# Kernel optimization log

Measured on AMD Instinct MI355X. Metric: run time of the kernel, lower is better.

The kernel has to match this reference:

```python
import jax, jax.numpy as jnp
import numpy as np

N_HEADS = 16
ROPE_BASE = 10000.0


def _rope_cos_sin(seq_len, head_dim, dtype):
    half = head_dim // 2
    inv_freq = 1.0 / (ROPE_BASE ** (jnp.arange(0, half, dtype=jnp.float32) / half))
    ang = jnp.arange(seq_len, dtype=jnp.float32)[:, None] * inv_freq[None, :]  # [S, half]
    cos = jnp.concatenate([jnp.cos(ang), jnp.cos(ang)], axis=-1).astype(dtype)  # [S, hd]
    sin = jnp.concatenate([jnp.sin(ang), jnp.sin(ang)], axis=-1).astype(dtype)
    return cos, sin


def _rotate_half(x):
    half = x.shape[-1] // 2
    return jnp.concatenate([-x[..., half:], x[..., :half]], axis=-1)


def setup_inputs() -> dict:
    key = jax.random.key(0)
    k1, k2, k3 = jax.random.split(key, 3)
    B, S, D = 2, 2048, 1024
    x = jax.random.normal(k1, (B, S, D), dtype=jnp.float32)
    w_qkv = jax.random.normal(k2, (D, 3 * D), dtype=jnp.float32) * (1.0 / np.sqrt(D))
    w_out = jax.random.normal(k3, (D, D), dtype=jnp.float32) * (1.0 / np.sqrt(D))
    return {"x": x, "w_qkv": w_qkv, "w_out": w_out}


def reference(x, w_qkv, w_out):
    B, S, D = x.shape
    H = N_HEADS
    hd = D // H
    scale = 1.0 / np.sqrt(hd)

    qkv = x @ w_qkv  # [B, S, 3D]
    q, k, v = jnp.split(qkv, 3, axis=-1)
    # [B, H, S, hd]
    q = q.reshape(B, S, H, hd).transpose(0, 2, 1, 3)
    k = k.reshape(B, S, H, hd).transpose(0, 2, 1, 3)
    v = v.reshape(B, S, H, hd).transpose(0, 2, 1, 3)

    cos, sin = _rope_cos_sin(S, hd, x.dtype)  # [S, hd]
    q = q * cos + _rotate_half(q) * sin
    k = k * cos + _rotate_half(k) * sin

    scores = jnp.einsum("bhqd,bhkd->bhqk", q, k) * scale  # [B, H, S, S]
    causal = jnp.tril(jnp.ones((S, S), dtype=bool))
    scores = jnp.where(causal[None, None, :, :], scores, -jnp.inf)

    probs = jax.nn.softmax(scores.astype(jnp.float32), axis=-1).astype(q.dtype)
    out = jnp.einsum("bhqk,bhkd->bhqd", probs, v)  # [B, H, S, hd]
    out = out.transpose(0, 2, 1, 3).reshape(B, S, D)
    return out @ w_out
```

## Files before the change

kernel.cpp:

```cpp
#include <hip/hip_runtime.h>
#include <math.h>
#include <type_traits>

#define B_  2
#define S_  2048
#define D_  1024
#define H_  16

typedef short bf16x8 __attribute__((ext_vector_type(8)));
typedef short bf16x4 __attribute__((ext_vector_type(4)));
typedef float f32x4  __attribute__((ext_vector_type(4)));

__device__ __forceinline__ short f2bf(float f) {
    unsigned u = __builtin_bit_cast(unsigned, f);
    u += 0x7FFFu + ((u >> 16) & 1u);
    return (short)(u >> 16);
}
__device__ __forceinline__ float bf2f(short s) {
    unsigned u = ((unsigned)(unsigned short)s) << 16;
    return __builtin_bit_cast(float, u);
}

__device__ __forceinline__ void gload16(const short* g, const void* l) {
    __builtin_amdgcn_global_load_lds(
        (const __attribute__((address_space(1))) void*)g,
        (__attribute__((address_space(3))) void*)l, 16, 0, 0);
}

__global__ __launch_bounds__(256) void cvt_bf16_kernel(
    const float* __restrict__ in, short* __restrict__ out)
{
    int i = (blockIdx.x * 256 + threadIdx.x) * 8;
    float4 a = *(const float4*)(in + i);
    float4 b = *(const float4*)(in + i + 4);
    bf16x8 o;
    o[0] = f2bf(a.x); o[1] = f2bf(a.y); o[2] = f2bf(a.z); o[3] = f2bf(a.w);
    o[4] = f2bf(b.x); o[5] = f2bf(b.y); o[6] = f2bf(b.z); o[7] = f2bf(b.w);
    *(bf16x8*)(out + i) = o;
}

__global__ __launch_bounds__(256) void transpose_cvt_kernel(
    const float* __restrict__ in, short* __restrict__ out, int K, int N)
{
    __shared__ short t[64][72];
    const int k0 = blockIdx.y * 64, n0 = blockIdx.x * 64;
    const int r = threadIdx.x >> 2;
    const int c = (threadIdx.x & 3) * 16;
    const float* src = in + (size_t)(k0 + r) * N + n0 + c;
#pragma unroll
    for (int i = 0; i < 16; ++i) t[c + i][r] = f2bf(src[i]);
    __syncthreads();
    short* dst = out + (size_t)(n0 + r) * K + k0 + c;
    *(bf16x8*)(dst)     = *(const bf16x8*)&t[r][c];
    *(bf16x8*)(dst + 8) = *(const bf16x8*)&t[r][c + 8];
}

__global__ __launch_bounds__(256) void rope_tab_kernel(float2* __restrict__ tab)
{
    int idx = blockIdx.x * 256 + threadIdx.x;
    int j = idx & 31, s = idx >> 5;
    float inv = powf(10000.0f, -(float)j * (1.0f / 32.0f));
    float sn, cs;
    sincosf((float)s * inv, &sn, &cs);
    tab[idx] = make_float2(cs, sn);
}

__global__ __launch_bounds__(256) void gemm_bt_f32(
    const short* __restrict__ A, const short* __restrict__ Bt,
    float* __restrict__ C, int M, int N, int K)
{
    __shared__ short smem[18432];

    const int tid  = threadIdx.x;
    const int wave = tid >> 6, lane = tid & 63;
    const int quad = lane >> 4, l16 = lane & 15;
    const int wm = wave >> 1, wn = wave & 1;
    const int row0 = blockIdx.y * 128, col0 = blockIdx.x * 64;

    f32x4 acc[4][2];
#pragma unroll
    for (int mi = 0; mi < 4; ++mi)
#pragma unroll
        for (int ni = 0; ni < 2; ++ni) acc[mi][ni] = (f32x4)0.f;

    const int sr = tid >> 2;
    const int sc = (tid & 3) * 8;
    const short* a0 = A  + (size_t)(row0 + sr) * K + sc;
    const short* a1 = A  + (size_t)(row0 + 64 + sr) * K + sc;
    const short* b0 = Bt + (size_t)(col0 + sr) * K + sc;

    auto stage = [&](int b, int kt) {
        char* l = (char*)(smem + b * 6144) + wave * 1024;
        const int k0 = kt * 32;
        gload16(a0 + k0, l);
        gload16(a1 + k0, l + 4096);
        gload16(b0 + k0, l + 8192);
    };

    const int NT = K >> 5;
    stage(0, 0);
    stage(1, 1);
    int bufid = 0;
    for (int kt = 0; kt < NT; ++kt) {
        if (kt + 1 < NT) { asm volatile("s_waitcnt vmcnt(3)" ::: "memory"); }
        else             { asm volatile("s_waitcnt vmcnt(0)" ::: "memory"); }
        __builtin_amdgcn_s_barrier();
        __builtin_amdgcn_sched_barrier(0);
        if (kt + 2 < NT) {
            int nb = bufid + 2; if (nb >= 3) nb -= 3;
            stage(nb, kt + 2);
        }

        const short* As = smem + bufid * 6144;
        const short* Bs = As + 4096;
        bf16x8 af[4], bfr[2];
#pragma unroll
        for (int mi = 0; mi < 4; ++mi)
            af[mi] = *(const bf16x8*)(As + (wm * 64 + mi * 16 + l16) * 32 + quad * 8);
#pragma unroll
        for (int ni = 0; ni < 2; ++ni)
            bfr[ni] = *(const bf16x8*)(Bs + (wn * 32 + ni * 16 + l16) * 32 + quad * 8);
#pragma unroll
        for (int mi = 0; mi < 4; ++mi)
#pragma unroll
            for (int ni = 0; ni < 2; ++ni)
                acc[mi][ni] = __builtin_amdgcn_mfma_f32_16x16x32_bf16(
                    af[mi], bfr[ni], acc[mi][ni], 0, 0, 0);

        bufid = (bufid + 1 == 3) ? 0 : bufid + 1;
    }

#pragma unroll
    for (int mi = 0; mi < 4; ++mi)
#pragma unroll
        for (int ni = 0; ni < 2; ++ni)
#pragma unroll
            for (int r = 0; r < 4; ++r) {
                int row = row0 + wm * 64 + mi * 16 + quad * 4 + r;
                int col = col0 + wn * 32 + ni * 16 + l16;
                C[(size_t)row * N + col] = acc[mi][ni][r];
            }
}

__global__ __launch_bounds__(256) void gemm_qkv(
    const short* __restrict__ A, const short* __restrict__ Bt,
    const float2* __restrict__ tab,
    short* __restrict__ Qb, short* __restrict__ Kb, short* __restrict__ Vt)
{
    const int K = 1024;
    extern __shared__ short smem[];
    short* Sc = smem;

    const int tid  = threadIdx.x;
    const int wave = tid >> 6, lane = tid & 63;
    const int quad = lane >> 4, l16 = lane & 15;
    const int wm = wave >> 1, wn = wave & 1;
    const int row0 = blockIdx.y * 128, col0 = blockIdx.x * 128;

    f32x4 acc[4][4];
#pragma unroll
    for (int mi = 0; mi < 4; ++mi)
#pragma unroll
        for (int ni = 0; ni < 4; ++ni) acc[mi][ni] = (f32x4)0.f;

    const int sr = tid >> 2;
    const int sc = (tid & 3) * 8;
    const short* a0 = A  + (size_t)(row0 + sr) * K + sc;
    const short* a1 = A  + (size_t)(row0 + 64 + sr) * K + sc;
    const short* b0 = Bt + (size_t)(col0 + sr) * K + sc;
    const short* b1 = Bt + (size_t)(col0 + 64 + sr) * K + sc;

    auto stage = [&](int b, int kt) {
        char* l = (char*)(smem + b * 8192) + wave * 1024;
        const int k0 = kt * 32;
        gload16(a0 + k0, l);
        gload16(a1 + k0, l + 4096);
        gload16(b0 + k0, l + 8192);
        gload16(b1 + k0, l + 12288);
    };

    const int NT = K >> 5;
    stage(0, 0);
    stage(1, 1);
    int bufid = 0;
    for (int kt = 0; kt < NT; ++kt) {
        if (kt + 1 < NT) { asm volatile("s_waitcnt vmcnt(4)" ::: "memory"); }
        else             { asm volatile("s_waitcnt vmcnt(0)" ::: "memory"); }
        __builtin_amdgcn_s_barrier();
        __builtin_amdgcn_sched_barrier(0);
        if (kt + 2 < NT) {
            int nb = bufid + 2; if (nb >= 3) nb -= 3;
            stage(nb, kt + 2);
        }

        const short* As = smem + bufid * 8192;
        const short* Bs = As + 4096;
        bf16x8 af[4], bfr[4];
#pragma unroll
        for (int mi = 0; mi < 4; ++mi)
            af[mi] = *(const bf16x8*)(As + (wm * 64 + mi * 16 + l16) * 32 + quad * 8);
#pragma unroll
        for (int ni = 0; ni < 4; ++ni)
            bfr[ni] = *(const bf16x8*)(Bs + (wn * 64 + ni * 16 + l16) * 32 + quad * 8);
#pragma unroll
        for (int mi = 0; mi < 4; ++mi)
#pragma unroll
            for (int ni = 0; ni < 4; ++ni)
                acc[mi][ni] = __builtin_amdgcn_mfma_f32_16x16x32_bf16(
                    af[mi], bfr[ni], acc[mi][ni], 0, 0, 0);

        bufid = (bufid + 1 == 3) ? 0 : bufid + 1;
    }

    __syncthreads();

    const int sec  = (col0 + wn * 64) >> 6;
    const int h    = sec & 15;
    const int kind = sec >> 4;
    short* myS = Sc + wave * 4608;

    const int mrow0 = row0 + wm * 64;
    const int b  = mrow0 >> 11;
    const int bh = b * 16 + h;
    const int sbase = mrow0 & (S_ - 1);

    if (kind < 2) {
#pragma unroll
        for (int mi = 0; mi < 4; ++mi) {
#pragma unroll
            for (int r = 0; r < 4; ++r) {
                int sl = mi * 16 + quad * 4 + r;
                int s = sbase + sl;
#pragma unroll
                for (int ni = 0; ni < 2; ++ni) {
                    int j = ni * 16 + l16;
                    float2 t = tab[s * 32 + j];
                    float lo = acc[mi][ni][r], hi = acc[mi][ni + 2][r];
                    float olo = lo * t.x - hi * t.y;
                    float ohi = hi * t.x + lo * t.y;
                    if (kind == 0) { olo *= 0.125f; ohi *= 0.125f; }
                    myS[sl * 72 + j]      = f2bf(olo);
                    myS[sl * 72 + 32 + j] = f2bf(ohi);
                }
            }
        }
        const int rl = lane >> 3;
        const int cl = (lane & 7) * 8;
        short* dst = (kind == 0 ? Qb : Kb);
#pragma unroll
        for (int p = 0; p < 8; ++p) {
            int rr = p * 8 + rl;
            bf16x8 v = *(const bf16x8*)&myS[rr * 72 + cl];
            *(bf16x8*)(dst + ((size_t)bh * S_ + sbase + rr) * 64 + cl) = v;
        }
    } else {
#pragma unroll
        for (int mi = 0; mi < 4; ++mi)
#pragma unroll
            for (int ni = 0; ni < 4; ++ni) {
                bf16x4 p;
                p[0] = f2bf(acc[mi][ni][0]);
                p[1] = f2bf(acc[mi][ni][1]);
                p[2] = f2bf(acc[mi][ni][2]);
                p[3] = f2bf(acc[mi][ni][3]);
                *(bf16x4*)&myS[(ni * 16 + l16) * 72 + mi * 16 + quad * 4] = p;
            }
        const int rl = lane >> 3;
        const int cl = (lane & 7) * 8;
#pragma unroll
        for (int p = 0; p < 8; ++p) {
            int dd = p * 8 + rl;
            bf16x8 v = *(const bf16x8*)&myS[dd * 72 + cl];
            *(bf16x8*)(Vt + ((size_t)bh * 64 + dd) * S_ + sbase + cl) = v;
        }
    }
}

__global__ __launch_bounds__(128, 4) void attn_kernel(
    const short* __restrict__ Qb, const short* __restrict__ Kb,
    const short* __restrict__ Vt, short* __restrict__ Opart,
    float* __restrict__ lpart)
{
    __shared__ short Ps[64][72];

    const int lin = blockIdx.x;
    const int xcd = lin & 7;
    const int j   = lin >> 3;
    const int bh   = xcd * 4 + (j & 3);
    const int task = j >> 2;

    const int g = task < 8 ? 0 : task < 24 ? 1 : task < 48 ? 2 : 3;
    const int cumstart = g == 0 ? 0 : g == 1 ? 8 : g == 2 ? 24 : 48;
    const int idx = task - cumstart;
    const int qd = idx / (g + 1);
    const int qb = 8 * g + qd;
    const int c  = idx - qd * (g + 1);
    const int t0 = c * 8;
    const int t1 = min(qb, c * 8 + 7);

    const int wave = threadIdx.x >> 6, lane = threadIdx.x & 63;
    const int quad = lane >> 4, l16 = lane & 15;
    const size_t head64 = (size_t)bh * S_ * 64;

    bf16x8 qf[2][2];
#pragma unroll
    for (int m = 0; m < 2; ++m) {
        const short* qrow = Qb + head64
            + (size_t)(qb * 64 + wave * 32 + m * 16 + l16) * 64 + quad * 8;
        qf[m][0] = *(const bf16x8*)(qrow);
        qf[m][1] = *(const bf16x8*)(qrow + 32);
    }

    bf16x8 ones;
#pragma unroll
    for (int i = 0; i < 8; ++i) ones[i] = (short)0x3F80;

    f32x4 lacc[2] = {(f32x4)0.f, (f32x4)0.f};
    f32x4 oacc[2][4];
#pragma unroll
    for (int m = 0; m < 2; ++m)
#pragma unroll
        for (int nt = 0; nt < 4; ++nt) oacc[m][nt] = (f32x4)0.f;

    for (int t = t0; t <= t1; ++t) {
        const short* kb = Kb + head64 + (size_t)t * 64 * 64;
        const short* vb = Vt + head64 + t * 64;

        f32x4 s4[2][4];
#pragma unroll
        for (int nt = 0; nt < 4; ++nt) {
            const short* kr = kb + (nt * 16 + l16) * 64 + quad * 8;
            bf16x8 k0 = *(const bf16x8*)kr;
            bf16x8 k1 = *(const bf16x8*)(kr + 32);
#pragma unroll
            for (int m = 0; m < 2; ++m) {
                f32x4 a = (f32x4)0.f;
                a = __builtin_amdgcn_mfma_f32_16x16x32_bf16(k0, qf[m][0], a, 0, 0, 0);
                a = __builtin_amdgcn_mfma_f32_16x16x32_bf16(k1, qf[m][1], a, 0, 0, 0);
                s4[m][nt] = a;
            }
        }

        if (t == qb) {
#pragma unroll
            for (int m = 0; m < 2; ++m)
#pragma unroll
                for (int nt = 0; nt < 4; ++nt)
#pragma unroll
                    for (int r = 0; r < 4; ++r)
                        if (nt * 16 + quad * 4 + r > wave * 32 + m * 16 + l16)
                            s4[m][nt][r] = -INFINITY;
        }

#pragma unroll
        for (int m = 0; m < 2; ++m)
#pragma unroll
            for (int nt = 0; nt < 4; ++nt) {
                bf16x4 p;
#pragma unroll
                for (int r = 0; r < 4; ++r)
                    p[r] = f2bf(__expf(s4[m][nt][r] - 8.0f));
                *(bf16x4*)&Ps[wave * 32 + m * 16 + l16][nt * 16 + quad * 4] = p;
            }

        bf16x8 pa[2][2];
#pragma unroll
        for (int m = 0; m < 2; ++m) {
            pa[m][0] = *(const bf16x8*)&Ps[wave * 32 + m * 16 + l16][quad * 8];
            pa[m][1] = *(const bf16x8*)&Ps[wave * 32 + m * 16 + l16][32 + quad * 8];
        }

#pragma unroll
        for (int m = 0; m < 2; ++m) {
            lacc[m] = __builtin_amdgcn_mfma_f32_16x16x32_bf16(pa[m][0], ones, lacc[m], 0, 0, 0);
            lacc[m] = __builtin_amdgcn_mfma_f32_16x16x32_bf16(pa[m][1], ones, lacc[m], 0, 0, 0);
        }

#pragma unroll
        for (int nt = 0; nt < 4; ++nt) {
            const short* vrp = vb + (size_t)(nt * 16 + l16) * S_ + quad * 8;
            bf16x8 vb0 = *(const bf16x8*)vrp;
            bf16x8 vb1 = *(const bf16x8*)(vrp + 32);
#pragma unroll
            for (int m = 0; m < 2; ++m) {
                oacc[m][nt] = __builtin_amdgcn_mfma_f32_16x16x32_bf16(
                    pa[m][0], vb0, oacc[m][nt], 0, 0, 0);
                oacc[m][nt] = __builtin_amdgcn_mfma_f32_16x16x32_bf16(
                    pa[m][1], vb1, oacc[m][nt], 0, 0, 0);
            }
        }
    }

    const int pidx = bh * 80 + task;
#pragma unroll
    for (int m = 0; m < 2; ++m)
#pragma unroll
        for (int r = 0; r < 4; ++r) {
            int ql = wave * 32 + m * 16 + quad * 4 + r;
            short* orow = Opart + (size_t)pidx * 4096 + ql * 64;
#pragma unroll
            for (int nt = 0; nt < 4; ++nt)
                orow[nt * 16 + l16] = f2bf(oacc[m][nt][r]);
            if (l16 == 0)
                lpart[(size_t)pidx * 64 + ql] = lacc[m][r];
        }
}

__global__ __launch_bounds__(256) void combine_kernel(
    const short* __restrict__ Opart, const float* __restrict__ lpart,
    short* __restrict__ attnb)
{
    const int qb = blockIdx.x, bh = blockIdx.y;
    const int g = qb >> 3, nch = g + 1;
    const int cbase = bh * 80 + nch * (qb - 4 * g);
    const int q = threadIdx.x >> 2;
    const int dg = (threadIdx.x & 3) * 16;

    float lsum = 0.f;
    float acc[16];
#pragma unroll
    for (int i = 0; i < 16; ++i) acc[i] = 0.f;

    for (int cc = 0; cc < nch; ++cc) {
        lsum += lpart[(size_t)(cbase + cc) * 64 + q];
        const short* src = Opart + (size_t)(cbase + cc) * 4096 + q * 64 + dg;
        bf16x8 o0 = *(const bf16x8*)src;
        bf16x8 o1 = *(const bf16x8*)(src + 8);
#pragma unroll
        for (int i = 0; i < 8; ++i) {
            acc[i]     += bf2f(o0[i]);
            acc[i + 8] += bf2f(o1[i]);
        }
    }
    float inv = 1.0f / lsum;
    const int b = bh >> 4, h = bh & 15;
    bf16x8 r0, r1;
#pragma unroll
    for (int i = 0; i < 8; ++i) {
        r0[i] = f2bf(acc[i] * inv);
        r1[i] = f2bf(acc[i + 8] * inv);
    }
    short* dst = attnb + (size_t)(b * S_ + qb * 64 + q) * 1024 + h * 64 + dg;
    *(bf16x8*)dst       = r0;
    *(bf16x8*)(dst + 8) = r1;
}

extern "C" void kernel_launch(void* const* d_in, const int* in_sizes, int n_in,
                              void* d_out, int out_size, void* d_ws, size_t ws_size,
                              hipStream_t stream)
{
    const float* x     = (const float*)d_in[0];
    const float* w_qkv = (const float*)d_in[1];
    const float* w_out = (const float*)d_in[2];
    float* out = (float*)d_out;

    short* Qb   = (short*)d_ws;
    short* Kb   = Qb   + (size_t)4096 * 1024;
    short* Vt   = Kb   + (size_t)4096 * 1024;
    short* Xb   = Vt   + (size_t)4096 * 1024;
    short* Wqt  = Xb   + (size_t)4096 * 1024;
    short* Wot  = Wqt  + (size_t)3072 * 1024;
    float2* tab = (float2*)(Wot + (size_t)1024 * 1024);
    short* Opart = (short*)(tab + 2048 * 32);
    float* lbuf  = (float*)(Opart + (size_t)2560 * 4096);
    short* attnb = Xb;

    cvt_bf16_kernel<<<(4096 * 1024 / 8) / 256, 256, 0, stream>>>(x, Xb);
    transpose_cvt_kernel<<<dim3(3072 / 64, 1024 / 64), 256, 0, stream>>>(
        w_qkv, Wqt, 1024, 3072);
    transpose_cvt_kernel<<<dim3(1024 / 64, 1024 / 64), 256, 0, stream>>>(
        w_out, Wot, 1024, 1024);
    rope_tab_kernel<<<(2048 * 32) / 256, 256, 0, stream>>>(tab);

    gemm_qkv<<<dim3(3072 / 128, 4096 / 128), 256, 49152, stream>>>(
        Xb, Wqt, tab, Qb, Kb, Vt);

    attn_kernel<<<2560, 128, 0, stream>>>(Qb, Kb, Vt, Opart, lbuf);

    combine_kernel<<<dim3(32, 32), 256, 0, stream>>>(Opart, lbuf, attnb);

    gemm_bt_f32<<<dim3(1024 / 64, 4096 / 128), 256, 0, stream>>>(
        attnb, Wot, out, 4096, 1024, 1024);
}
```

Measured before the change: 216.4 us.

## Share double-buffered K/V LDS tiles across 128-row query blocks in attention

The attention kernel now gives each block 128 query rows over 4 waves instead of 64 rows over 2, so every K/V tile serves twice as many queries. K and V tiles are staged into swizzled, double-buffered LDS with async global-to-LDS loads, and the next tile is prefetched while the current one is computed. Task decomposition, partial buffer indexing and the combine kernel are rewritten for the new 128-row blocking. In exchange the block uses more LDS and registers, adds barriers per tile, and launches half as many blocks.

```diff
diff --git a/kernel.cpp b/kernel.cpp
--- a/kernel.cpp
+++ b/kernel.cpp
@@ -276,12 +276,14 @@
     }
 }
 
-__global__ __launch_bounds__(128, 4) void attn_kernel(
+__global__ __launch_bounds__(256, 3) void attn_kernel(
     const short* __restrict__ Qb, const short* __restrict__ Kb,
     const short* __restrict__ Vt, short* __restrict__ Opart,
     float* __restrict__ lpart)
 {
-    __shared__ short Ps[64][72];
+    __shared__ short Ks[2][64 * 64];
+    __shared__ short Vs[2][64 * 64];
+    __shared__ short Ps[128][72];
 
     const int lin = blockIdx.x;
     const int xcd = lin & 7;
@@ -289,24 +291,26 @@
     const int bh   = xcd * 4 + (j & 3);
     const int task = j >> 2;
 
-    const int g = task < 8 ? 0 : task < 24 ? 1 : task < 48 ? 2 : 3;
-    const int cumstart = g == 0 ? 0 : g == 1 ? 8 : g == 2 ? 24 : 48;
+    const int g = task < 4 ? 0 : task < 12 ? 1 : task < 24 ? 2 : 3;
+    const int cumstart = g == 0 ? 0 : g == 1 ? 4 : g == 2 ? 12 : 24;
     const int idx = task - cumstart;
     const int qd = idx / (g + 1);
-    const int qb = 8 * g + qd;
+    const int qb = 4 * g + qd;
     const int c  = idx - qd * (g + 1);
     const int t0 = c * 8;
-    const int t1 = min(qb, c * 8 + 7);
+    const int t1 = min(2 * qb + 1, c * 8 + 7);
 
     const int wave = threadIdx.x >> 6, lane = threadIdx.x & 63;
     const int quad = lane >> 4, l16 = lane & 15;
+    const int subr  = lane >> 3;
+    const int chunk = (lane & 7) ^ subr;
     const size_t head64 = (size_t)bh * S_ * 64;
 
     bf16x8 qf[2][2];
 #pragma unroll
     for (int m = 0; m < 2; ++m) {
         const short* qrow = Qb + head64
-            + (size_t)(qb * 64 + wave * 32 + m * 16 + l16) * 64 + quad * 8;
+            + (size_t)(qb * 128 + wave * 32 + m * 16 + l16) * 64 + quad * 8;
         qf[m][0] = *(const bf16x8*)(qrow);
         qf[m][1] = *(const bf16x8*)(qrow + 32);
     }
@@ -315,6 +319,18 @@
 #pragma unroll
     for (int i = 0; i < 8; ++i) ones[i] = (short)0x3F80;
 
+    auto stage = [&](int buf, int t) {
+        const short* kt = Kb + head64 + (size_t)(t * 64 + wave * 16) * 64;
+        const short* vt = Vt + head64 + (size_t)(wave * 16) * S_ + t * 64;
+        char* kl = (char*)(Ks[buf]) + wave * 2048;
+        char* vl = (char*)(Vs[buf]) + wave * 2048;
+#pragma unroll
+        for (int g2 = 0; g2 < 2; ++g2) {
+            gload16(kt + (g2 * 8 + subr) * 64 + chunk * 8, kl + g2 * 1024);
+            gload16(vt + (size_t)(g2 * 8 + subr) * S_ + chunk * 8, vl + g2 * 1024);
+        }
+    };
+
     f32x4 lacc[2] = {(f32x4)0.f, (f32x4)0.f};
     f32x4 oacc[2][4];
 #pragma unroll
@@ -322,16 +338,26 @@
 #pragma unroll
         for (int nt = 0; nt < 4; ++nt) oacc[m][nt] = (f32x4)0.f;
 
+    stage(0, t0);
+    int buf = 0;
     for (int t = t0; t <= t1; ++t) {
-        const short* kb = Kb + head64 + (size_t)t * 64 * 64;
-        const short* vb = Vt + head64 + t * 64;
+        __builtin_amdgcn_s_barrier();
+        if (t < t1) stage(buf ^ 1, t + 1);
+        if (t < t1) { asm volatile("s_waitcnt vmcnt(4)" ::: "memory"); }
+        else        { asm volatile("s_waitcnt vmcnt(0)" ::: "memory"); }
+        __builtin_amdgcn_s_barrier();
+        __builtin_amdgcn_sched_barrier(0);
+
+        const short* kbuf = Ks[buf];
+        const short* vbuf = Vs[buf];
 
         f32x4 s4[2][4];
 #pragma unroll
         for (int nt = 0; nt < 4; ++nt) {
-            const short* kr = kb + (nt * 16 + l16) * 64 + quad * 8;
-            bf16x8 k0 = *(const bf16x8*)kr;
-            bf16x8 k1 = *(const bf16x8*)(kr + 32);
+            const int krow = nt * 16 + l16;
+            const int sw = krow & 7;
+            bf16x8 k0 = *(const bf16x8*)(kbuf + krow * 64 + ((quad ^ sw) << 3));
+            bf16x8 k1 = *(const bf16x8*)(kbuf + krow * 64 + (((quad + 4) ^ sw) << 3));
 #pragma unroll
             for (int m = 0; m < 2; ++m) {
                 f32x4 a = (f32x4)0.f;
@@ -341,15 +367,18 @@
             }
         }
 
-        if (t == qb) {
-#pragma unroll
-            for (int m = 0; m < 2; ++m)
+        if (t >= 2 * qb) {
+            const int kbase = (t - 2 * qb) * 64;
+#pragma unroll
+            for (int m = 0; m < 2; ++m) {
+                const int qq = wave * 32 + m * 16 + l16;
 #pragma unroll
                 for (int nt = 0; nt < 4; ++nt)
 #pragma unroll
                     for (int r = 0; r < 4; ++r)
-                        if (nt * 16 + quad * 4 + r > wave * 32 + m * 16 + l16)
+                        if (kbase + nt * 16 + quad * 4 + r > qq)
                             s4[m][nt][r] = -INFINITY;
+            }
         }
 
 #pragma unroll
@@ -378,31 +407,33 @@
 
 #pragma unroll
         for (int nt = 0; nt < 4; ++nt) {
-            const short* vrp = vb + (size_t)(nt * 16 + l16) * S_ + quad * 8;
-            bf16x8 vb0 = *(const bf16x8*)vrp;
-            bf16x8 vb1 = *(const bf16x8*)(vrp + 32);
+            const int vrow = nt * 16 + l16;
+            const int sw = vrow & 7;
+            bf16x8 v0 = *(const bf16x8*)(vbuf + vrow * 64 + ((quad ^ sw) << 3));
+            bf16x8 v1 = *(const bf16x8*)(vbuf + vrow * 64 + (((quad + 4) ^ sw) << 3));
 #pragma unroll
             for (int m = 0; m < 2; ++m) {
                 oacc[m][nt] = __builtin_amdgcn_mfma_f32_16x16x32_bf16(
-                    pa[m][0], vb0, oacc[m][nt], 0, 0, 0);
+                    pa[m][0], v0, oacc[m][nt], 0, 0, 0);
                 oacc[m][nt] = __builtin_amdgcn_mfma_f32_16x16x32_bf16(
-                    pa[m][1], vb1, oacc[m][nt], 0, 0, 0);
-            }
-        }
-    }
-
-    const int pidx = bh * 80 + task;
+                    pa[m][1], v1, oacc[m][nt], 0, 0, 0);
+            }
+        }
+        buf ^= 1;
+    }
+
+    const int pidx = bh * 40 + task;
 #pragma unroll
     for (int m = 0; m < 2; ++m)
 #pragma unroll
         for (int r = 0; r < 4; ++r) {
             int ql = wave * 32 + m * 16 + quad * 4 + r;
-            short* orow = Opart + (size_t)pidx * 4096 + ql * 64;
+            short* orow = Opart + (size_t)pidx * 8192 + ql * 64;
 #pragma unroll
             for (int nt = 0; nt < 4; ++nt)
                 orow[nt * 16 + l16] = f2bf(oacc[m][nt][r]);
             if (l16 == 0)
-                lpart[(size_t)pidx * 64 + ql] = lacc[m][r];
+                lpart[(size_t)pidx * 128 + ql] = lacc[m][r];
         }
 }
 
@@ -411,38 +442,37 @@
     short* __restrict__ attnb)
 {
     const int qb = blockIdx.x, bh = blockIdx.y;
-    const int g = qb >> 3, nch = g + 1;
-    const int cbase = bh * 80 + nch * (qb - 4 * g);
-    const int q = threadIdx.x >> 2;
-    const int dg = (threadIdx.x & 3) * 16;
+    const int g = qb >> 2, nch = g + 1;
+    const int cumstart = g == 0 ? 0 : g == 1 ? 4 : g == 2 ? 12 : 24;
+    const int cbase = bh * 40 + cumstart + (qb - 4 * g) * nch;
+    const int q = threadIdx.x >> 1;
+    const int dg = (threadIdx.x & 1) * 32;
 
     float lsum = 0.f;
-    float acc[16];
-#pragma unroll
-    for (int i = 0; i < 16; ++i) acc[i] = 0.f;
+    float acc[32];
+#pragma unroll
+    for (int i = 0; i < 32; ++i) acc[i] = 0.f;
 
     for (int cc = 0; cc < nch; ++cc) {
-        lsum += lpart[(size_t)(cbase + cc) * 64 + q];
-        const short* src = Opart + (size_t)(cbase + cc) * 4096 + q * 64 + dg;
-        bf16x8 o0 = *(const bf16x8*)src;
-        bf16x8 o1 = *(const bf16x8*)(src + 8);
-#pragma unroll
-        for (int i = 0; i < 8; ++i) {
-            acc[i]     += bf2f(o0[i]);
-            acc[i + 8] += bf2f(o1[i]);
+        lsum += lpart[(size_t)(cbase + cc) * 128 + q];
+        const short* src = Opart + (size_t)(cbase + cc) * 8192 + q * 64 + dg;
+#pragma unroll
+        for (int w = 0; w < 4; ++w) {
+            bf16x8 o = *(const bf16x8*)(src + w * 8);
+#pragma unroll
+            for (int i = 0; i < 8; ++i) acc[w * 8 + i] += bf2f(o[i]);
         }
     }
     float inv = 1.0f / lsum;
     const int b = bh >> 4, h = bh & 15;
-    bf16x8 r0, r1;
-#pragma unroll
-    for (int i = 0; i < 8; ++i) {
-        r0[i] = f2bf(acc[i] * inv);
-        r1[i] = f2bf(acc[i + 8] * inv);
-    }
-    short* dst = attnb + (size_t)(b * S_ + qb * 64 + q) * 1024 + h * 64 + dg;
-    *(bf16x8*)dst       = r0;
-    *(bf16x8*)(dst + 8) = r1;
+    short* dst = attnb + (size_t)(b * S_ + qb * 128 + q) * 1024 + h * 64 + dg;
+#pragma unroll
+    for (int w = 0; w < 4; ++w) {
+        bf16x8 r;
+#pragma unroll
+        for (int i = 0; i < 8; ++i) r[i] = f2bf(acc[w * 8 + i] * inv);
+        *(bf16x8*)(dst + w * 8) = r;
+    }
 }
 
 extern "C" void kernel_launch(void* const* d_in, const int* in_sizes, int n_in,
@@ -462,7 +492,7 @@
     short* Wot  = Wqt  + (size_t)3072 * 1024;
     float2* tab = (float2*)(Wot + (size_t)1024 * 1024);
     short* Opart = (short*)(tab + 2048 * 32);
-    float* lbuf  = (float*)(Opart + (size_t)2560 * 4096);
+    float* lbuf  = (float*)(Opart + (size_t)1280 * 8192);
     short* attnb = Xb;
 
     cvt_bf16_kernel<<<(4096 * 1024 / 8) / 256, 256, 0, stream>>>(x, Xb);
@@ -475,9 +505,9 @@
     gemm_qkv<<<dim3(3072 / 128, 4096 / 128), 256, 49152, stream>>>(
         Xb, Wqt, tab, Qb, Kb, Vt);
 
-    attn_kernel<<<2560, 128, 0, stream>>>(Qb, Kb, Vt, Opart, lbuf);
-
-    combine_kernel<<<dim3(32, 32), 256, 0, stream>>>(Opart, lbuf, attnb);
+    attn_kernel<<<1280, 256, 0, stream>>>(Qb, Kb, Vt, Opart, lbuf);
+
+    combine_kernel<<<dim3(16, 32), 256, 0, stream>>>(Opart, lbuf, attnb);
 
     gemm_bt_f32<<<dim3(1024 / 64, 4096 / 128), 256, 0, stream>>>(
         attnb, Wot, out, 4096, 1024, 1024);
```

Result: faster. 178.5 us (-17.5%).
